# Performance work log

Measured on AMD Instinct MI355X. Metric: run time of the kernel, lower is better.

## Reference

```python
import jax, jax.numpy as jnp
import numpy as np

B, S, DEC, ENC, ATTN = 64, 1024, 1024, 1024, 1024

def setup_inputs() -> dict:
    key = jax.random.key(0)
    k1, k2, k3, k4, k5 = jax.random.split(key, 5)
    hidden = jax.random.normal(k1, (B, DEC), dtype=jnp.float32)
    encoder_outputs = jax.random.normal(k2, (B, S, ENC), dtype=jnp.float32)
    # nn.Linear(dec+enc -> attn_dim): weight [attn, dec+enc], bias [attn]
    fan_in = DEC + ENC
    bound = 1.0 / np.sqrt(fan_in)
    W_attn = jax.random.uniform(k3, (ATTN, fan_in), dtype=jnp.float32, minval=-bound, maxval=bound)
    b_attn = jax.random.uniform(k4, (ATTN,), dtype=jnp.float32, minval=-bound, maxval=bound)
    # v = torch.rand(attn_dim) -> uniform [0,1)
    v = jax.random.uniform(k5, (ATTN,), dtype=jnp.float32)
    return {"hidden": hidden, "encoder_outputs": encoder_outputs,
            "W_attn": W_attn, "b_attn": b_attn, "v": v}

def reference(hidden, encoder_outputs, W_attn, b_attn, v):
    # hidden: [B, DEC], encoder_outputs: [B, S, ENC]
    b, s, _ = encoder_outputs.shape
    h = jnp.broadcast_to(hidden[:, None, :], (b, s, hidden.shape[-1]))
    combined = jnp.concatenate([h, encoder_outputs], axis=-1)        # [B, S, DEC+ENC]
    energy = jnp.tanh(jnp.einsum('bsf,af->bsa', combined, W_attn) + b_attn)  # [B, S, ATTN]
    scores = jnp.einsum('bsa,a->bs', energy, v)                      # [B, S]
    attn_weights = jax.nn.softmax(scores, axis=1)                    # [B, S]
    context = jnp.einsum('bs,bse->be', attn_weights, encoder_outputs)[:, None, :]  # [B, 1, ENC]
    return context
```

## Files before the change

kernel.cpp:

```cpp
#include <hip/hip_runtime.h>
#include <hip/hip_bf16.h>
#include <stdint.h>

#define NB 64
#define NS 1024
#define NE 1024
#define NA 1024
#define NF 2048
#define LDP 144

typedef __attribute__((ext_vector_type(8))) short   short8;
typedef __attribute__((ext_vector_type(4))) short   short4v;
typedef __attribute__((ext_vector_type(4))) float   f32x4;
typedef __attribute__((ext_vector_type(8))) __bf16  bf16x8;

__device__ __forceinline__ unsigned short f2bf(float x) {
  union { float f; unsigned u; } v; v.f = x;
  unsigned r = v.u + 0x7fffu + ((v.u >> 16) & 1u);
  return (unsigned short)(r >> 16);
}
__device__ __forceinline__ float bf2f(unsigned short h) {
  union { unsigned u; float f; } v; v.u = ((unsigned)h) << 16;
  return v.f;
}
__device__ __forceinline__ float tanh_fast(float x) {
  float e = __expf(2.0f * x);
  return 1.0f - __fdividef(2.0f, e + 1.0f);
}
__device__ __forceinline__ short8 pack8(float4 a, float4 b) {
  short8 h;
  h[0]=(short)f2bf(a.x); h[1]=(short)f2bf(a.y); h[2]=(short)f2bf(a.z); h[3]=(short)f2bf(a.w);
  h[4]=(short)f2bf(b.x); h[5]=(short)f2bf(b.y); h[6]=(short)f2bf(b.z); h[7]=(short)f2bf(b.w);
  return h;
}
__device__ __forceinline__ void gload_lds16(const void* g, void* l) {
  __builtin_amdgcn_global_load_lds((const __attribute__((address_space(1))) void*)g,
                                   (__attribute__((address_space(3))) void*)l, 16, 0, 0);
}

__global__ __launch_bounds__(256) void k_zero(float4* __restrict__ p, int n4) {
  int i = blockIdx.x * 256 + threadIdx.x;
  if (i < n4) { float4 z; z.x = z.y = z.z = z.w = 0.f; p[i] = z; }
}

__global__ __launch_bounds__(256) void k_conv_enc(const float4* __restrict__ src,
                                                  short8* __restrict__ dst, int n8) {
  int i = blockIdx.x * 256 + threadIdx.x;
  const int stride = gridDim.x * 256;
  for (; i < n8; i += stride) {
    float4 a = src[2 * i], b = src[2 * i + 1];
    dst[i] = pack8(a, b);
  }
}

__global__ __launch_bounds__(256) void k_conv_w(const float* __restrict__ W, short8* __restrict__ dst) {
  const int id = blockIdx.x * 256 + threadIdx.x;
  const int a = id >> 7, ku = id & 127;
  const float* s = W + (size_t)a * NF + 1024 + ku * 8;
  float4 x = *(const float4*)s;
  float4 y = *(const float4*)(s + 4);
  dst[id] = pack8(x, y);
}

__global__ __launch_bounds__(256) void k_u(const float* __restrict__ hidden,
                                           const float* __restrict__ W,
                                           const float* __restrict__ bias,
                                           float* __restrict__ u) {
  const int l = threadIdx.x & 63;
  const int w = threadIdx.x >> 6;
  const int a = (blockIdx.x >> 1) * 4 + w;
  const int bh = blockIdx.x & 1;
  const float* wrow = W + (size_t)a * NF;
  float4 wv[4];
  #pragma unroll
  for (int i = 0; i < 4; ++i) wv[i] = *(const float4*)(wrow + l * 4 + i * 256);
  const float ba = bias[a];
  for (int b = bh * 32; b < bh * 32 + 32; ++b) {
    const float* hrow = hidden + b * 1024;
    float s = 0.f;
    #pragma unroll
    for (int i = 0; i < 4; ++i) {
      float4 hv = *(const float4*)(hrow + l * 4 + i * 256);
      s += wv[i].x * hv.x + wv[i].y * hv.y + wv[i].z * hv.z + wv[i].w * hv.w;
    }
    #pragma unroll
    for (int m = 1; m < 64; m <<= 1) s += __shfl_xor(s, m);
    if (l == 0) u[b * NA + a] = s + ba;
  }
}

__global__ __launch_bounds__(512, 2) void k_main256(const unsigned short* __restrict__ Ab,
                                                    const unsigned short* __restrict__ Bb,
                                                    const float* __restrict__ u_,
                                                    const float* __restrict__ v_,
                                                    float* __restrict__ scores) {
  __shared__ __align__(16) char smem[2 * 65536];

  const int tid = threadIdx.x;
  const int l = tid & 63;
  const int w = tid >> 6;
  const int wr = w >> 2, wc = w & 3;
  const int d = blockIdx.x;
  const int xcd = d & 7, q = d >> 3;
  const int rt = xcd * 32 + (q >> 2);
  const int ct = q & 3;
  const int b = rt >> 2;
  const int lh = l >> 4, l15 = l & 15, l7 = l & 7;

  const int ssk = ((tid & 7) ^ ((tid >> 3) & 7)) * 8;
  const unsigned short* aS = Ab + (size_t)(rt * 256 + (tid >> 3)) * NE + ssk;
  const unsigned short* bS = Bb + (size_t)(ct * 256 + (tid >> 3)) * NE + ssk;
  const int wdst = w * 1024;

  f32x4 acc[8][4] = {};

#define STG_A(tt) do { \
    char* dst_ = smem + (((tt) & 1) << 16); \
    const unsigned short* a_ = aS + (size_t)(tt) * 64; \
    gload_lds16(a_,                    dst_ + wdst); \
    gload_lds16(a_ + (size_t) 64 * NE, dst_ +  64 * 128 + wdst); \
    gload_lds16(a_ + (size_t)128 * NE, dst_ + 128 * 128 + wdst); \
    gload_lds16(a_ + (size_t)192 * NE, dst_ + 192 * 128 + wdst); } while (0)
#define STG_B(tt) do { \
    char* dst_ = smem + (((tt) & 1) << 16) + 32768; \
    const unsigned short* b_ = bS + (size_t)(tt) * 64; \
    gload_lds16(b_,                    dst_ + wdst); \
    gload_lds16(b_ + (size_t) 64 * NE, dst_ +  64 * 128 + wdst); \
    gload_lds16(b_ + (size_t)128 * NE, dst_ + 128 * 128 + wdst); \
    gload_lds16(b_ + (size_t)192 * NE, dst_ + 192 * 128 + wdst); } while (0)

  STG_B(0); STG_A(0); STG_B(1); STG_A(1);

  bf16x8 areg[4][2], breg[4][2];

  for (int t = 0; t < 16; ++t) {
    if (t < 15) asm volatile("s_waitcnt vmcnt(8)" ::: "memory");
    else        asm volatile("s_waitcnt vmcnt(0)" ::: "memory");
    asm volatile("s_barrier" ::: "memory");

    const char* As = smem + ((t & 1) << 16);
    const char* Bs = As + 32768;

    #pragma unroll
    for (int rf = 0; rf < 4; ++rf)
      #pragma unroll
      for (int kh = 0; kh < 2; ++kh)
        areg[rf][kh] = *(const bf16x8*)(As + (wr * 128 + rf * 16 + l15) * 128
                                           + (((kh * 4 + lh) ^ l7) << 4));
    #pragma unroll
    for (int cf = 0; cf < 2; ++cf)
      #pragma unroll
      for (int kh = 0; kh < 2; ++kh)
        breg[cf][kh] = *(const bf16x8*)(Bs + (wc * 64 + cf * 16 + l15) * 128
                                           + (((kh * 4 + lh) ^ l7) << 4));
    __builtin_amdgcn_s_setprio(1);
    #pragma unroll
    for (int rf = 0; rf < 4; ++rf)
      #pragma unroll
      for (int cf = 0; cf < 2; ++cf)
        #pragma unroll
        for (int kh = 0; kh < 2; ++kh)
          acc[rf][cf] = __builtin_amdgcn_mfma_f32_16x16x32_bf16(areg[rf][kh], breg[cf][kh], acc[rf][cf], 0, 0, 0);
    __builtin_amdgcn_s_setprio(0);

    #pragma unroll
    for (int cf = 2; cf < 4; ++cf)
      #pragma unroll
      for (int kh = 0; kh < 2; ++kh)
        breg[cf][kh] = *(const bf16x8*)(Bs + (wc * 64 + cf * 16 + l15) * 128
                                           + (((kh * 4 + lh) ^ l7) << 4));
    __builtin_amdgcn_s_setprio(1);
    #pragma unroll
    for (int rf = 0; rf < 4; ++rf)
      #pragma unroll
      for (int cf = 2; cf < 4; ++cf)
        #pragma unroll
        for (int kh = 0; kh < 2; ++kh)
          acc[rf][cf] = __builtin_amdgcn_mfma_f32_16x16x32_bf16(areg[rf][kh], breg[cf][kh], acc[rf][cf], 0, 0, 0);
    __builtin_amdgcn_s_setprio(0);
    asm volatile("s_barrier" ::: "memory");

    if (t < 14) STG_B(t + 2);
    #pragma unroll
    for (int rf = 0; rf < 4; ++rf)
      #pragma unroll
      for (int kh = 0; kh < 2; ++kh)
        areg[rf][kh] = *(const bf16x8*)(As + (wr * 128 + (4 + rf) * 16 + l15) * 128
                                           + (((kh * 4 + lh) ^ l7) << 4));
    __builtin_amdgcn_s_setprio(1);
    #pragma unroll
    for (int rf = 0; rf < 4; ++rf)
      #pragma unroll
      for (int cf = 0; cf < 2; ++cf)
        #pragma unroll
        for (int kh = 0; kh < 2; ++kh)
          acc[4 + rf][cf] = __builtin_amdgcn_mfma_f32_16x16x32_bf16(areg[rf][kh], breg[cf][kh], acc[4 + rf][cf], 0, 0, 0);
    __builtin_amdgcn_s_setprio(0);
    asm volatile("s_barrier" ::: "memory");

    if (t < 14) STG_A(t + 2);
    __builtin_amdgcn_s_setprio(1);
    #pragma unroll
    for (int rf = 0; rf < 4; ++rf)
      #pragma unroll
      for (int cf = 2; cf < 4; ++cf)
        #pragma unroll
        for (int kh = 0; kh < 2; ++kh)
          acc[4 + rf][cf] = __builtin_amdgcn_mfma_f32_16x16x32_bf16(areg[rf][kh], breg[cf][kh], acc[4 + rf][cf], 0, 0, 0);
    __builtin_amdgcn_s_setprio(0);
  }
#undef STG_A
#undef STG_B

  const int colb = ct * 256 + wc * 64 + l15;
  float uv[4], vv[4];
  #pragma unroll
  for (int cf = 0; cf < 4; ++cf) {
    const int c = colb + cf * 16;
    uv[cf] = u_[b * NA + c];
    vv[cf] = v_[c];
  }
  #pragma unroll
  for (int rf = 0; rf < 8; ++rf) {
    #pragma unroll
    for (int reg = 0; reg < 4; ++reg) {
      float sacc = 0.f;
      #pragma unroll
      for (int cf = 0; cf < 4; ++cf)
        sacc += tanh_fast(acc[rf][cf][reg] + uv[cf]) * vv[cf];
      sacc += __shfl_xor(sacc, 1);
      sacc += __shfl_xor(sacc, 2);
      sacc += __shfl_xor(sacc, 4);
      sacc += __shfl_xor(sacc, 8);
      if (l15 == 0) {
        const int m = rt * 256 + wr * 128 + rf * 16 + lh * 4 + reg;
        atomicAdd(&scores[m], sacc);
      }
    }
  }
}

template <int ACONV, int BCONV>
__global__ __launch_bounds__(256) void k_main_rs(const void* __restrict__ Asrc,
                                                 const void* __restrict__ Bsrc,
                                                 const float* __restrict__ u_,
                                                 const float* __restrict__ v_,
                                                 float* __restrict__ scores) {
  __shared__ __align__(16) char smemf[2 * 128 * LDP];
  char* As = smemf;
  char* Bs = smemf + 128 * LDP;
  const int tid = threadIdx.x;
  const int l = tid & 63;
  const int w = tid >> 6;
  const int wr = w >> 1, wc = w & 1;
  const int d = blockIdx.x;
  const int rt = (d & 7) * 64 + (d >> 6);
  const int ct = (d >> 3) & 7;
  const int b = rt >> 3;
  const int l7 = l & 7, lh = l >> 4, l15 = l & 15;
  const int srow = w * 8 + (l >> 3);
  f32x4 acc[4][4] = {};
  for (int kt = 0; kt < 16; ++kt) {
    const int k0 = kt * 64;
    __syncthreads();
    #pragma unroll
    for (int r = 0; r < 4; ++r) {
      const int row = r * 32 + srow;
      short8 val;
      if constexpr (ACONV) {
        const float* s = (const float*)Asrc + (size_t)(rt * 128 + row) * NE + k0 + l7 * 8;
        val = pack8(*(const float4*)s, *(const float4*)(s + 4));
      } else {
        val = *(const short8*)((const unsigned short*)Asrc + (size_t)(rt * 128 + row) * NE + k0 + l7 * 8);
      }
      *(short8*)(As + row * LDP + l7 * 16) = val;
    }
    #pragma unroll
    for (int r = 0; r < 4; ++r) {
      const int row = r * 32 + srow;
      short8 val;
      if constexpr (BCONV) {
        const float* s = (const float*)Bsrc + (size_t)(ct * 128 + row) * NF + 1024 + k0 + l7 * 8;
        val = pack8(*(const float4*)s, *(const float4*)(s + 4));
      } else {
        val = *(const short8*)((const unsigned short*)Bsrc + (size_t)(ct * 128 + row) * NE + k0 + l7 * 8);
      }
      *(short8*)(Bs + row * LDP + l7 * 16) = val;
    }
    __syncthreads();
    #pragma unroll
    for (int ks = 0; ks < 2; ++ks) {
      bf16x8 af[4], bfr[4];
      const int ku = (ks * 4 + lh) * 16;
      #pragma unroll
      for (int f = 0; f < 4; ++f) {
        af[f]  = *(const bf16x8*)(As + (wr * 64 + f * 16 + l15) * LDP + ku);
        bfr[f] = *(const bf16x8*)(Bs + (wc * 64 + f * 16 + l15) * LDP + ku);
      }
      #pragma unroll
      for (int i = 0; i < 4; ++i)
        #pragma unroll
        for (int jj = 0; jj < 4; ++jj)
          acc[i][jj] = __builtin_amdgcn_mfma_f32_16x16x32_bf16(af[i], bfr[jj], acc[i][jj], 0, 0, 0);
    }
  }
  const int colb = ct * 128 + wc * 64 + l15;
  float uv[4], vv[4];
  #pragma unroll
  for (int jj = 0; jj < 4; ++jj) {
    const int c = colb + jj * 16;
    uv[jj] = u_[b * NA + c];
    vv[jj] = v_[c];
  }
  #pragma unroll
  for (int i = 0; i < 4; ++i) {
    #pragma unroll
    for (int reg = 0; reg < 4; ++reg) {
      float sacc = 0.f;
      #pragma unroll
      for (int jj = 0; jj < 4; ++jj)
        sacc += tanh_fast(acc[i][jj][reg] + uv[jj]) * vv[jj];
      sacc += __shfl_xor(sacc, 1);
      sacc += __shfl_xor(sacc, 2);
      sacc += __shfl_xor(sacc, 4);
      sacc += __shfl_xor(sacc, 8);
      if (l15 == 0) {
        const int m = rt * 128 + wr * 64 + i * 16 + lh * 4 + reg;
        atomicAdd(&scores[m], sacc);
      }
    }
  }
}

__global__ __launch_bounds__(256) void k_softmax(float* __restrict__ sc) {
  const int b = blockIdx.x, t = threadIdx.x;
  float4 x = *(float4*)(sc + b * NS + t * 4);
  float mx = fmaxf(fmaxf(x.x, x.y), fmaxf(x.z, x.w));
  #pragma unroll
  for (int m = 1; m < 64; m <<= 1) mx = fmaxf(mx, __shfl_xor(mx, m));
  __shared__ float rmax[4], rsum[4];
  if ((t & 63) == 0) rmax[t >> 6] = mx;
  __syncthreads();
  mx = fmaxf(fmaxf(rmax[0], rmax[1]), fmaxf(rmax[2], rmax[3]));
  float e0 = __expf(x.x - mx), e1 = __expf(x.y - mx);
  float e2 = __expf(x.z - mx), e3 = __expf(x.w - mx);
  float sm = e0 + e1 + e2 + e3;
  #pragma unroll
  for (int m = 1; m < 64; m <<= 1) sm += __shfl_xor(sm, m);
  if ((t & 63) == 0) rsum[t >> 6] = sm;
  __syncthreads();
  sm = rsum[0] + rsum[1] + rsum[2] + rsum[3];
  const float inv = 1.0f / sm;
  float4 o; o.x = e0 * inv; o.y = e1 * inv; o.z = e2 * inv; o.w = e3 * inv;
  *(float4*)(sc + b * NS + t * 4) = o;
}

template <int CONV>
__global__ __launch_bounds__(256) void k_ctx(const void* __restrict__ encsrc,
                                             const float* __restrict__ wgt,
                                             float* __restrict__ ctx) {
  const int b = blockIdx.x >> 4, scn = blockIdx.x & 15;
  const int t = threadIdx.x;
  float a0 = 0.f, a1 = 0.f, a2 = 0.f, a3 = 0.f;
  for (int s = scn * 64; s < scn * 64 + 64; ++s) {
    const float wv = wgt[b * NS + s];
    const size_t base = ((size_t)(b * NS + s)) * NE + t * 4;
    if constexpr (CONV) {
      float4 x = *((const float4*)((const float*)encsrc + base));
      a0 += wv * x.x; a1 += wv * x.y; a2 += wv * x.z; a3 += wv * x.w;
    } else {
      short4v hv = *(const short4v*)((const unsigned short*)encsrc + base);
      a0 += wv * bf2f((unsigned short)hv[0]);
      a1 += wv * bf2f((unsigned short)hv[1]);
      a2 += wv * bf2f((unsigned short)hv[2]);
      a3 += wv * bf2f((unsigned short)hv[3]);
    }
  }
  float* c = ctx + b * NE + t * 4;
  atomicAdd(c + 0, a0); atomicAdd(c + 1, a1);
  atomicAdd(c + 2, a2); atomicAdd(c + 3, a3);
}

__global__ __launch_bounds__(256) void k_out(const float* __restrict__ ctx,
                                             float* __restrict__ out) {
  const int i = blockIdx.x * 256 + threadIdx.x;
  float4 x = *(const float4*)(ctx + i * 4);
  *(float4*)(out + i * 4) = x;
}

extern "C" void kernel_launch(void* const* d_in, const int* in_sizes, int n_in,
                              void* d_out, int out_size, void* d_ws, size_t ws_size,
                              hipStream_t stream) {
  const float* hidden = (const float*)d_in[0];
  const float* enc    = (const float*)d_in[1];
  const float* W      = (const float*)d_in[2];
  const float* bias   = (const float*)d_in[3];
  const float* v      = (const float*)d_in[4];
  (void)in_sizes; (void)n_in; (void)out_size;

  char* ws = (char*)d_ws;
  const size_t T0 = (4ull << 20) + (128ull << 20);
  const size_t T1 = (3ull << 20);
  const int tier = (ws_size >= T0) ? 0 : ((ws_size >= T1) ? 1 : 2);

  unsigned short* Wb   = (unsigned short*)ws;
  unsigned short* encb = (unsigned short*)(ws + (4ull << 20));
  float* u_  = (tier < 2) ? (float*)(ws + (2ull << 20)) : (float*)ws;
  float* sc  = u_ + NB * NA;
  float* ctx = sc + NB * NS;

  k_u<<<512, 256, 0, stream>>>(hidden, W, bias, u_);
  k_zero<<<128, 256, 0, stream>>>((float4*)sc, (NB * NS + NB * NE) / 4);

  if (tier == 0) {
    k_conv_w<<<512, 256, 0, stream>>>(W, (short8*)Wb);
    k_conv_enc<<<2048, 256, 0, stream>>>((const float4*)enc, (short8*)encb, NB * NS * NE / 8);
    k_main256<<<1024, 512, 0, stream>>>(encb, Wb, u_, v, sc);
  } else if (tier == 1) {
    k_conv_w<<<512, 256, 0, stream>>>(W, (short8*)Wb);
    k_main_rs<1, 0><<<4096, 256, 0, stream>>>(enc, Wb, u_, v, sc);
  } else {
    k_main_rs<1, 1><<<4096, 256, 0, stream>>>(enc, W, u_, v, sc);
  }

  k_softmax<<<64, 256, 0, stream>>>(sc);
  if (tier == 0) k_ctx<0><<<1024, 256, 0, stream>>>(encb, sc, ctx);
  else           k_ctx<1><<<1024, 256, 0, stream>>>(enc, sc, ctx);
  k_out<<<64, 256, 0, stream>>>(ctx, (float*)d_out);
}
```

Before: 281.9 us.

## Interleave split global-to-LDS loads across MFMA phases of the GEMM main loop

The A and B tile loads are split into half-tile chunks (A02/A13, B01/B23) and spread across the four MFMA phases of each k-iteration. The B23 half for the next step is issued during the current step. Explicit barriers, lgkmcnt waits and sched_barriers pin LDS reads ahead of each MFMA burst, and the vmcnt wait moves to the end of the iteration. The aim is smoother memory traffic that overlaps better with matrix-core work, at the cost of more barriers per iteration and a tighter buffer-reuse schedule.

```diff
diff --git a/kernel.cpp b/kernel.cpp
--- a/kernel.cpp
+++ b/kernel.cpp
@@ -114,30 +114,35 @@
 
   f32x4 acc[8][4] = {};
 
-#define STG_A(tt) do { \
+#define STG_A02(tt) do { \
     char* dst_ = smem + (((tt) & 1) << 16); \
     const unsigned short* a_ = aS + (size_t)(tt) * 64; \
     gload_lds16(a_,                    dst_ + wdst); \
+    gload_lds16(a_ + (size_t)128 * NE, dst_ + 128 * 128 + wdst); } while (0)
+#define STG_A13(tt) do { \
+    char* dst_ = smem + (((tt) & 1) << 16); \
+    const unsigned short* a_ = aS + (size_t)(tt) * 64; \
     gload_lds16(a_ + (size_t) 64 * NE, dst_ +  64 * 128 + wdst); \
-    gload_lds16(a_ + (size_t)128 * NE, dst_ + 128 * 128 + wdst); \
     gload_lds16(a_ + (size_t)192 * NE, dst_ + 192 * 128 + wdst); } while (0)
-#define STG_B(tt) do { \
+#define STG_B01(tt) do { \
     char* dst_ = smem + (((tt) & 1) << 16) + 32768; \
     const unsigned short* b_ = bS + (size_t)(tt) * 64; \
     gload_lds16(b_,                    dst_ + wdst); \
-    gload_lds16(b_ + (size_t) 64 * NE, dst_ +  64 * 128 + wdst); \
+    gload_lds16(b_ + (size_t) 64 * NE, dst_ +  64 * 128 + wdst); } while (0)
+#define STG_B23(tt) do { \
+    char* dst_ = smem + (((tt) & 1) << 16) + 32768; \
+    const unsigned short* b_ = bS + (size_t)(tt) * 64; \
     gload_lds16(b_ + (size_t)128 * NE, dst_ + 128 * 128 + wdst); \
     gload_lds16(b_ + (size_t)192 * NE, dst_ + 192 * 128 + wdst); } while (0)
 
-  STG_B(0); STG_A(0); STG_B(1); STG_A(1);
+  STG_A02(0); STG_B01(0); STG_A13(0); STG_B23(0);
+  STG_A02(1); STG_B01(1); STG_A13(1);
+  asm volatile("s_waitcnt vmcnt(6)" ::: "memory");
+  asm volatile("s_barrier" ::: "memory");
 
   bf16x8 areg[4][2], breg[4][2];
 
   for (int t = 0; t < 16; ++t) {
-    if (t < 15) asm volatile("s_waitcnt vmcnt(8)" ::: "memory");
-    else        asm volatile("s_waitcnt vmcnt(0)" ::: "memory");
-    asm volatile("s_barrier" ::: "memory");
-
     const char* As = smem + ((t & 1) << 16);
     const char* Bs = As + 32768;
 
@@ -153,6 +158,10 @@
       for (int kh = 0; kh < 2; ++kh)
         breg[cf][kh] = *(const bf16x8*)(Bs + (wc * 64 + cf * 16 + l15) * 128
                                            + (((kh * 4 + lh) ^ l7) << 4));
+    if (t < 15) STG_B23(t + 1);
+    asm volatile("s_barrier" ::: "memory");
+    asm volatile("s_waitcnt lgkmcnt(0)" ::: "memory");
+    __builtin_amdgcn_sched_barrier(0);
     __builtin_amdgcn_s_setprio(1);
     #pragma unroll
     for (int rf = 0; rf < 4; ++rf)
@@ -162,6 +171,7 @@
         for (int kh = 0; kh < 2; ++kh)
           acc[rf][cf] = __builtin_amdgcn_mfma_f32_16x16x32_bf16(areg[rf][kh], breg[cf][kh], acc[rf][cf], 0, 0, 0);
     __builtin_amdgcn_s_setprio(0);
+    asm volatile("s_barrier" ::: "memory");
 
     #pragma unroll
     for (int cf = 2; cf < 4; ++cf)
@@ -169,6 +179,10 @@
       for (int kh = 0; kh < 2; ++kh)
         breg[cf][kh] = *(const bf16x8*)(Bs + (wc * 64 + cf * 16 + l15) * 128
                                            + (((kh * 4 + lh) ^ l7) << 4));
+    if (t < 14) STG_A02(t + 2);
+    asm volatile("s_barrier" ::: "memory");
+    asm volatile("s_waitcnt lgkmcnt(0)" ::: "memory");
+    __builtin_amdgcn_sched_barrier(0);
     __builtin_amdgcn_s_setprio(1);
     #pragma unroll
     for (int rf = 0; rf < 4; ++rf)
@@ -180,13 +194,16 @@
     __builtin_amdgcn_s_setprio(0);
     asm volatile("s_barrier" ::: "memory");
 
-    if (t < 14) STG_B(t + 2);
     #pragma unroll
     for (int rf = 0; rf < 4; ++rf)
       #pragma unroll
       for (int kh = 0; kh < 2; ++kh)
         areg[rf][kh] = *(const bf16x8*)(As + (wr * 128 + (4 + rf) * 16 + l15) * 128
                                            + (((kh * 4 + lh) ^ l7) << 4));
+    if (t < 14) STG_B01(t + 2);
+    asm volatile("s_barrier" ::: "memory");
+    asm volatile("s_waitcnt lgkmcnt(0)" ::: "memory");
+    __builtin_amdgcn_sched_barrier(0);
     __builtin_amdgcn_s_setprio(1);
     #pragma unroll
     for (int rf = 0; rf < 4; ++rf)
@@ -198,7 +215,7 @@
     __builtin_amdgcn_s_setprio(0);
     asm volatile("s_barrier" ::: "memory");
 
-    if (t < 14) STG_A(t + 2);
+    if (t < 14) STG_A13(t + 2);
     __builtin_amdgcn_s_setprio(1);
     #pragma unroll
     for (int rf = 0; rf < 4; ++rf)
@@ -208,9 +225,14 @@
         for (int kh = 0; kh < 2; ++kh)
           acc[4 + rf][cf] = __builtin_amdgcn_mfma_f32_16x16x32_bf16(areg[rf][kh], breg[cf][kh], acc[4 + rf][cf], 0, 0, 0);
     __builtin_amdgcn_s_setprio(0);
-  }
-#undef STG_A
-#undef STG_B
+    if (t < 14)       asm volatile("s_waitcnt vmcnt(6)" ::: "memory");
+    else if (t == 14) asm volatile("s_waitcnt vmcnt(0)" ::: "memory");
+    asm volatile("s_barrier" ::: "memory");
+  }
+#undef STG_A02
+#undef STG_A13
+#undef STG_B01
+#undef STG_B23
 
   const int colb = ct * 256 + wc * 64 + l15;
   float uv[4], vv[4];
```

Result: no change. 283.2 us (+0.5%).
